# Optimization experiments

Measured on AMD Instinct MI355X. Metric: run time of the kernel, lower is better.

## Reference

```python
import jax, jax.numpy as jnp
import numpy as np

H = 256   # lstm2 hidden size
D_IN = 512  # lstm2 input size (256 fed-back out + 256 audio)
BN_EPS = 1e-5


def _lstm_cell(x, h, c, Wih, Whh, bih, bhh):
    # torch gate order: i, f, g, o
    z = x @ Wih.T + h @ Whh.T + bih + bhh  # (B, 4H)
    i, f, g, o = jnp.split(z, 4, axis=-1)
    i = jax.nn.sigmoid(i)
    f = jax.nn.sigmoid(f)
    g = jnp.tanh(g)
    o = jax.nn.sigmoid(o)
    c = f * c + i * g
    h = o * jnp.tanh(c)
    return h, c


def setup_inputs() -> dict:
    key = jax.random.key(0)
    ks = jax.random.split(key, 16)
    B, T, L = 256, 512, 16
    s = 0.05
    inp = {
        "rt": jax.random.normal(ks[0], (B, H), jnp.float32),
        "audio": jax.random.normal(ks[1], (B, T, H), jnp.float32),
        "s_rt": jax.random.normal(ks[2], (B, L, H), jnp.float32),
        # lstm2 layer 0
        "W_ih_l0": jax.random.normal(ks[3], (4 * H, D_IN), jnp.float32) * s,
        "W_hh_l0": jax.random.normal(ks[4], (4 * H, H), jnp.float32) * s,
        "b_ih_l0": jax.random.normal(ks[5], (4 * H,), jnp.float32) * s,
        "b_hh_l0": jax.random.normal(ks[6], (4 * H,), jnp.float32) * s,
        # lstm2 layer 1
        "W_ih_l1": jax.random.normal(ks[7], (4 * H, H), jnp.float32) * s,
        "W_hh_l1": jax.random.normal(ks[8], (4 * H, H), jnp.float32) * s,
        "b_ih_l1": jax.random.normal(ks[9], (4 * H,), jnp.float32) * s,
        "b_hh_l1": jax.random.normal(ks[10], (4 * H,), jnp.float32) * s,
        # rt_linear head: Linear(256,128) -> BN(128) -> ReLU -> Linear(128,6)
        "W1": jax.random.normal(ks[11], (128, H), jnp.float32) * s,
        "b1": jax.random.normal(ks[12], (128,), jnp.float32) * s,
        "gamma": jnp.ones((128,), jnp.float32),
        "beta": jnp.zeros((128,), jnp.float32),
        "W2": jax.random.normal(ks[13], (6, 128), jnp.float32) * s,
        "b2": jax.random.normal(ks[14], (6,), jnp.float32) * s,
        "max_len": 0,
    }
    return inp


def reference(rt, audio, s_rt,
              W_ih_l0, W_hh_l0, b_ih_l0, b_hh_l0,
              W_ih_l1, W_hh_l1, b_ih_l1, b_hh_l1,
              W1, b1, gamma, beta, W2, b2, max_len):
    B, T, _ = audio.shape
    prev_out = jnp.mean(s_rt, axis=1)  # (B, 256): torch.mean(s_rt, dim=1)
    h1 = c1 = h2 = c2 = jnp.zeros((B, H), audio.dtype)

    def step(carry, a_t):
        prev_out, h1, c1, h2, c2 = carry
        x = jnp.concatenate([prev_out, a_t], axis=-1)  # (B, 512)
        h1n, c1n = _lstm_cell(x, h1, c1, W_ih_l0, W_hh_l0, b_ih_l0, b_hh_l0)
        h2n, c2n = _lstm_cell(h1n, h2, c2, W_ih_l1, W_hh_l1, b_ih_l1, b_hh_l1)
        return (h2n, h1n, c1n, h2n, c2n), h2n

    audio_tm = jnp.transpose(audio, (1, 0, 2))  # (T, B, 256) time-major
    _, out_tm = jax.lax.scan(step, (prev_out, h1, c1, h2, c2), audio_tm)
    out = jnp.transpose(out_tm, (1, 0, 2)).reshape(-1, H)  # (B*T, 256)

    # rt_linear head, BatchNorm1d in training mode (batch stats)
    y = out @ W1.T + b1  # (B*T, 128)
    mu = jnp.mean(y, axis=0)
    var = jnp.var(y, axis=0)
    y = (y - mu) * jax.lax.rsqrt(var + BN_EPS) * gamma + beta
    y = jax.nn.relu(y)
    y = y @ W2.T + b2  # (B*T, 6)
    return y.reshape(B, T, -1)
```

## Files before the change

kernel.cpp:

```cpp
#include <hip/hip_runtime.h>
#include <stdint.h>

typedef unsigned int u32;
typedef unsigned short u16;
typedef unsigned long long u64;
typedef _Float16 f16;
typedef _Float16 h2_t __attribute__((ext_vector_type(2)));
typedef _Float16 f16x4 __attribute__((ext_vector_type(4)));
typedef _Float16 f16x8 __attribute__((ext_vector_type(8)));
typedef float f32x4 __attribute__((ext_vector_type(4)));
typedef float f32x16 __attribute__((ext_vector_type(16)));
typedef u32 u32x4 __attribute__((ext_vector_type(4)));

#define TT 512
#define NF 128
#define NTOT (256 * TT)

#define OFF_WA0   0u
#define OFF_WA1   1572864u
#define OFF_WAH   2621440u
#define OFF_GSUM  2883584u
#define OFF_GSQ   2884096u
#define OFF_CTR   2884608u
#define OFF_GH1   2886656u
#define OFF_GH2   3017728u
#define OFF_Y     3148800u

__device__ __forceinline__ float sigf(float x) { return 1.0f / (1.0f + __expf(-x)); }
__device__ __forceinline__ float tanh_fast(float x) { return 1.0f - 2.0f / (__expf(2.0f * x) + 1.0f); }

__global__ void prep_kernel(const float* __restrict__ Wih0, const float* __restrict__ Whh0,
                            const float* __restrict__ Wih1, const float* __restrict__ Whh1,
                            const float* __restrict__ W1,
                            f16* __restrict__ WA0, f16* __restrict__ WA1, f16* __restrict__ WAH,
                            float* __restrict__ gz, u32* __restrict__ ctr) {
    int idx = blockIdx.x * 256 + threadIdx.x;
    const int n0 = 786432, n1 = 524288, n2 = 131072;
    if (idx < n0) {
        int u = idx >> 9, r9 = idx & 511;
        int lane = r9 >> 3, j = r9 & 7;
        int ks = u % 6; u /= 6;
        int wv = u & 7, w = u >> 3;
        int lr = lane & 31, h = lane >> 5;
        int r = ((lr >> 3) << 8) + 8 * w + (lr & 7);
        int seg = ks >> 1, sig = ks & 1;
        int c = 256 * seg + 32 * wv + 16 * sig + 8 * h + j;
        float v = (c < 512) ? Wih0[r * 512 + c] : Whh0[r * 256 + (c - 512)];
        WA0[idx] = (f16)v;
    } else if (idx < n0 + n1) {
        int i2 = idx - n0;
        int lane = (i2 >> 3) & 63, j = i2 & 7;
        int ks = (i2 >> 9) & 3, wv = (i2 >> 11) & 7, w = i2 >> 14;
        int lr = lane & 31, h = lane >> 5;
        int r = ((lr >> 3) << 8) + 8 * w + (lr & 7);
        int sig = ks & 1;
        int c = 32 * wv + 16 * sig + 8 * h + j;
        float v = (ks >> 1) ? Whh1[r * 256 + c] : Wih1[r * 256 + c];
        WA1[i2] = (f16)v;
    } else if (idx < n0 + n1 + n2) {
        int i2 = idx - n0 - n1;
        int u = i2 >> 9, r9 = i2 & 511;
        int lane = r9 >> 3, j = r9 & 7;
        int ks = u & 7, w = u >> 3;
        int m = lane & 15, hh = lane >> 4;
        int k = 32 * ks + 8 * hh + j;
        float v = (m < 4) ? W1[(4 * w + m) * 256 + k] : 0.f;
        WAH[i2] = (f16)v;
    } else if (idx < n0 + n1 + n2 + 256) {
        gz[idx - n0 - n1 - n2] = 0.f;
    } else if (idx < n0 + n1 + n2 + 256 + 512) {
        ctr[idx - n0 - n1 - n2 - 256] = 0u;
    }
}

#define MFMA32L(A, BP, C) (C) = __builtin_amdgcn_mfma_f32_32x32x16_f16( \
    __builtin_bit_cast(f16x8, (A)), __builtin_bit_cast(f16x8, *(const uint4*)(BP)), (C), 0, 0, 0)
#define MFMA32R(A, B, C) (C) = __builtin_amdgcn_mfma_f32_32x32x16_f16( \
    __builtin_bit_cast(f16x8, (A)), __builtin_bit_cast(f16x8, (B)), (C), 0, 0, 0)

#define ZZWR(KW, C) do { \
    f32x4 v0_ = {(C)[0], (C)[1], (C)[2], (C)[3]};    *(f32x4*)&zz[KW][n32][4 * h32] = v0_; \
    f32x4 v1_ = {(C)[4], (C)[5], (C)[6], (C)[7]};    *(f32x4*)&zz[KW][n32][8 + 4 * h32] = v1_; \
    f32x4 v2_ = {(C)[8], (C)[9], (C)[10], (C)[11]};  *(f32x4*)&zz[KW][n32][16 + 4 * h32] = v2_; \
    f32x4 v3_ = {(C)[12], (C)[13], (C)[14], (C)[15]}; *(f32x4*)&zz[KW][n32][24 + 4 * h32] = v3_; } while (0)

#define GATHER2(F0, F1, P0, P1) asm volatile( \
    "global_load_dwordx4 %0, %2, off sc0 sc1\n\t" \
    "global_load_dwordx4 %1, %3, off sc0 sc1\n\t" \
    "s_waitcnt vmcnt(0)" \
    : "=&v"(F0), "=&v"(F1) : "v"(P0), "v"(P1) : "memory")

#define PUBX4(PTR, DATA) asm volatile( \
    "global_store_dwordx4 %0, %1, off sc0 sc1" :: "v"(PTR), "v"(DATA) : "memory")

#define HEAD_BODY(TIDX) do { \
    f32x4 C_ = {}; \
    _Pragma("unroll") \
    for (int ks_ = 0; ks_ < 8; ++ks_) \
        C_ = __builtin_amdgcn_mfma_f32_16x16x32_f16( \
            __builtin_bit_cast(f16x8, ah[ks_]), \
            __builtin_bit_cast(f16x8, \
                *(const uint4*)&Xh2[wv * 16 + (lane & 15)][32 * ks_ + 8 * ((lane >> 4) & 3)]), \
            C_, 0, 0, 0); \
    if (lane < 16) { \
        float y0 = C_[0] + b1s[0], y1 = C_[1] + b1s[1]; \
        float y2 = C_[2] + b1s[2], y3 = C_[3] + b1s[3]; \
        ys0 += y0; yq0 += y0 * y0; ys1 += y1; yq1 += y1 * y1; \
        ys2 += y2; yq2 += y2 * y2; ys3 += y3; yq3 += y3 * y3; \
        f16x4 yp; yp[0] = (f16)y0; yp[1] = (f16)y1; yp[2] = (f16)y2; yp[3] = (f16)y3; \
        int b_ = wv * 16 + lane; \
        ((u64*)ybuf)[((size_t)(g * 32 + b_) * 512 + (TIDX)) * 32 + w] = __builtin_bit_cast(u64, yp); \
    } } while (0)

#define CELL_PUB(BCS, CSTATE, SRC) do { \
    float z0 = BCS[cj], z1 = BCS[8 + cj], z2 = BCS[16 + cj], z3 = BCS[24 + cj]; \
    _Pragma("unroll") \
    for (int kw_ = 0; kw_ < 8; ++kw_) { \
        z0 += zz[kw_][cb][cj];      z1 += zz[kw_][cb][8 + cj]; \
        z2 += zz[kw_][cb][16 + cj]; z3 += zz[kw_][cb][24 + cj]; \
    } \
    float c_ = sigf(z1) * (CSTATE) + sigf(z0) * tanh_fast(z2); \
    (CSTATE) = c_; \
    f16 hf_ = (f16)(sigf(z3) * tanh_fast(c_)); \
    u32 hb_ = (u32)__builtin_bit_cast(u16, hf_); \
    u32 p01_ = hb_ | ((u32)__shfl_xor((int)hb_, 1, 64) << 16); \
    u32 p23_ = (u32)__shfl_xor((int)p01_, 2, 64); \
    u32 p45_ = (u32)__shfl_xor((int)p01_, 4, 64); \
    u32 p67_ = (u32)__shfl_xor((int)p23_, 4, 64); \
    if (cj == 0) { \
        u32x4 word_ = {p01_, p23_, p45_, p67_}; \
        PUBX4((void*)((SRC) + ((cb << 5) + w) * 2), word_); \
    } } while (0)

#define FUNNEL_SYNC(LF, CTRP, T) do { \
    asm volatile("s_waitcnt vmcnt(0)" ::: "memory"); \
    if (lane == 0) \
        __hip_atomic_fetch_add(&(LF), 1u, __ATOMIC_RELAXED, __HIP_MEMORY_SCOPE_WORKGROUP); \
    if (wv == 7 && lane == 0) { \
        int gu_ = 0; \
        while (__hip_atomic_load(&(LF), __ATOMIC_RELAXED, __HIP_MEMORY_SCOPE_WORKGROUP) < 4u * (T) \
               && ++gu_ < 100000000) {} \
        __hip_atomic_fetch_add((CTRP), 1u, __ATOMIC_RELAXED, __HIP_MEMORY_SCOPE_AGENT); \
        gu_ = 0; \
        while (__hip_atomic_load((CTRP), __ATOMIC_RELAXED, __HIP_MEMORY_SCOPE_AGENT) < 32u * (T) \
               && ++gu_ < 100000000) {} \
    } } while (0)

__global__ __launch_bounds__(512) void lstm_group_kernel(
    const float* __restrict__ audio, const float* __restrict__ s_rt,
    const uint4* __restrict__ WA0, const uint4* __restrict__ WA1, const uint4* __restrict__ WAH,
    const float* __restrict__ bih0, const float* __restrict__ bhh0,
    const float* __restrict__ bih1, const float* __restrict__ bhh1,
    const float* __restrict__ b1, u32* __restrict__ ctr,
    u64* __restrict__ gh1u, u64* __restrict__ gh2u,
    f16* __restrict__ ybuf, float* __restrict__ gsum, float* __restrict__ gsq)
{
    __shared__ __align__(16) f16 Xa[32][264];
    __shared__ __align__(16) f16 Xh2[32][264];
    __shared__ float zz[8][32][36];
    __shared__ float bc0s[32], bc1s[32], b1s[4];
    __shared__ u32 lflag[2];
    __shared__ float pad_[2700];

    const int tid = threadIdx.x;
    const int w = blockIdx.x >> 3;
    const int g = blockIdx.x & 7;
    const int wv = tid >> 6;
    const int lane = tid & 63;
    const int n32 = lane & 31;
    const int h32 = (lane >> 5) & 1;
    const int ct = tid - 256;
    const int cb = ct >> 3, cj = ct & 7;
    const int bg = tid >> 6, aq = tid & 63;

    if (tid == 0) { volatile float* vp = pad_; vp[0] = 0.f; lflag[0] = 0u; lflag[1] = 0u; }

    u32* const ctr1 = ctr + (g * 2 + 0) * 32;
    u32* const ctr2 = ctr + (g * 2 + 1) * 32;
    u64* const src1 = gh1u + (size_t)g * 2048;
    u64* const src2 = gh2u + (size_t)g * 2048;
    const size_t gbase = (size_t)n32 * 64 + 8 * wv + 2 * h32;
    const float4* const a4 = (const float4*)audio;

    uint4 a0[6], a1[4], ah[8] = {};
    #pragma unroll
    for (int ks = 0; ks < 6; ++ks) a0[ks] = WA0[((w * 8 + wv) * 6 + ks) * 64 + lane];
    #pragma unroll
    for (int ks = 0; ks < 4; ++ks) a1[ks] = WA1[((w * 8 + wv) * 4 + ks) * 64 + lane];
    if (wv < 2) {
        #pragma unroll
        for (int ks = 0; ks < 8; ++ks) ah[ks] = WAH[(w * 8 + ks) * 64 + lane];
    }

    if (tid < 32) {
        int r = ((tid >> 3) << 8) + 8 * w + (tid & 7);
        bc0s[tid] = bih0[r] + bhh0[r];
        bc1s[tid] = bih1[r] + bhh1[r];
    }
    if (tid < 4) b1s[tid] = b1[4 * w + tid];

    for (int it = tid; it < 32 * 256; it += 512) {
        int b = it >> 8, c = it & 255;
        const float* sp = s_rt + ((size_t)(32 * g + b) * 16) * 256 + c;
        float s = 0.f;
        #pragma unroll
        for (int l = 0; l < 16; ++l) s += sp[l * 256];
        Xh2[b][c] = (f16)(s * 0.0625f);
        Xa[b][c] = (f16)audio[((size_t)(32 * g + b) * 512) * 256 + c];
    }
    float4 av[8];
    if (wv < 4) {
        #pragma unroll
        for (int s = 0; s < 8; ++s)
            av[s] = a4[(size_t)(32 * g + 8 * bg + s) * 32768 + 64 + aq];
    }
    __syncthreads();

    u32x4 f20 = *(const u32x4*)&Xh2[n32][32 * wv + 8 * h32];
    u32x4 f21 = *(const u32x4*)&Xh2[n32][32 * wv + 16 + 8 * h32];
    u32x4 f10 = {0, 0, 0, 0}, f11 = {0, 0, 0, 0};
    f32x16 aAcc = {};
    MFMA32L(a0[2], &Xa[n32][32 * wv + 8 * h32], aAcc);
    MFMA32L(a0[3], &Xa[n32][32 * wv + 16 + 8 * h32], aAcc);

    float c1 = 0.f, c2 = 0.f;
    float ys0 = 0, ys1 = 0, ys2 = 0, ys3 = 0, yq0 = 0, yq1 = 0, yq2 = 0, yq3 = 0;

    for (int t = 0; t < TT; ++t) {
        const u32 T = (u32)(t + 1);
        MFMA32R(a0[0], f20, aAcc);
        MFMA32R(a0[1], f21, aAcc);
        ZZWR(wv, aAcc);
        __syncthreads();

        f32x16 Dacc = {};
        if (wv >= 4) {
            CELL_PUB(bc0s, c1, src1);
            if (t > 0) { MFMA32R(a1[2], f20, Dacc); MFMA32R(a1[3], f21, Dacc); }
            FUNNEL_SYNC(lflag[0], ctr1, T);
        } else {
            if (t > 0) { MFMA32R(a1[2], f20, Dacc); MFMA32R(a1[3], f21, Dacc); }
            if (wv < 2 && t > 0) HEAD_BODY(t - 1);
            if (t + 1 < TT) {
                #pragma unroll
                for (int s = 0; s < 8; ++s) {
                    h2_t p0_; p0_.x = (f16)av[s].x; p0_.y = (f16)av[s].y;
                    h2_t p1_; p1_.x = (f16)av[s].z; p1_.y = (f16)av[s].w;
                    uint2 pv_;
                    pv_.x = __builtin_bit_cast(u32, p0_);
                    pv_.y = __builtin_bit_cast(u32, p1_);
                    *(uint2*)&Xa[8 * bg + s][4 * aq] = pv_;
                }
            }
        }
        __syncthreads();

        GATHER2(f10, f11, (const void*)(src1 + gbase), (const void*)(src1 + gbase + 4));
        if (wv < 4 && t + 2 < TT) {
            #pragma unroll
            for (int s = 0; s < 8; ++s)
                av[s] = a4[(size_t)(32 * g + 8 * bg + s) * 32768 + (size_t)(t + 2) * 64 + aq];
        }
        MFMA32R(a1[0], f10, Dacc);
        MFMA32R(a1[1], f11, Dacc);
        ZZWR(wv, Dacc);
        __syncthreads();

        aAcc = (f32x16){};
        if (wv >= 4) {
            CELL_PUB(bc1s, c2, src2);
            if (t + 1 < TT) {
                MFMA32L(a0[2], &Xa[n32][32 * wv + 8 * h32], aAcc);
                MFMA32L(a0[3], &Xa[n32][32 * wv + 16 + 8 * h32], aAcc);
                MFMA32R(a0[4], f10, aAcc);
                MFMA32R(a0[5], f11, aAcc);
            }
            FUNNEL_SYNC(lflag[1], ctr2, T);
        } else {
            if (t + 1 < TT) {
                MFMA32L(a0[2], &Xa[n32][32 * wv + 8 * h32], aAcc);
                MFMA32L(a0[3], &Xa[n32][32 * wv + 16 + 8 * h32], aAcc);
                MFMA32R(a0[4], f10, aAcc);
                MFMA32R(a0[5], f11, aAcc);
            }
        }
        __syncthreads();

        GATHER2(f20, f21, (const void*)(src2 + gbase), (const void*)(src2 + gbase + 4));
        *(u32x4*)&Xh2[n32][32 * wv + 8 * h32] = f20;
        *(u32x4*)&Xh2[n32][32 * wv + 16 + 8 * h32] = f21;
    }
    __syncthreads();
    if (wv < 2) HEAD_BODY(TT - 1);
    if (wv < 2 && lane < 16) {
        #pragma unroll
        for (int m = 8; m >= 1; m >>= 1) {
            ys0 += __shfl_xor(ys0, m, 64); ys1 += __shfl_xor(ys1, m, 64);
            ys2 += __shfl_xor(ys2, m, 64); ys3 += __shfl_xor(ys3, m, 64);
            yq0 += __shfl_xor(yq0, m, 64); yq1 += __shfl_xor(yq1, m, 64);
            yq2 += __shfl_xor(yq2, m, 64); yq3 += __shfl_xor(yq3, m, 64);
        }
        if (lane == 0) {
            atomicAdd(&gsum[4 * w + 0], ys0); atomicAdd(&gsum[4 * w + 1], ys1);
            atomicAdd(&gsum[4 * w + 2], ys2); atomicAdd(&gsum[4 * w + 3], ys3);
            atomicAdd(&gsq[4 * w + 0], yq0); atomicAdd(&gsq[4 * w + 1], yq1);
            atomicAdd(&gsq[4 * w + 2], yq2); atomicAdd(&gsq[4 * w + 3], yq3);
        }
    }
}

__global__ __launch_bounds__(256) void head_kernel(
    const f16* __restrict__ ybuf, const float* __restrict__ gsum, const float* __restrict__ gsq,
    const float* __restrict__ gamma, const float* __restrict__ beta,
    const float* __restrict__ W2, const float* __restrict__ b2,
    float* __restrict__ out)
{
    __shared__ float sc[NF], sh[NF], W2s[6 * NF], b2s[6];
    const int tid = threadIdx.x;
    if (tid < NF) {
        const float invN = 1.f / (float)NTOT;
        float mu = gsum[tid] * invN;
        float var = gsq[tid] * invN - mu * mu;
        float iv = rsqrtf(var + 1e-5f);
        float s = gamma[tid] * iv;
        sc[tid] = s;
        sh[tid] = beta[tid] - mu * s;
    }
    for (int i = tid; i < 6 * NF; i += 256) W2s[i] = W2[i];
    if (tid < 6) b2s[tid] = b2[tid];
    __syncthreads();

    size_t n = (size_t)blockIdx.x * 256 + tid;
    const h2_t* yr = (const h2_t*)(ybuf + n * NF);
    float a0 = b2s[0], a1 = b2s[1], a2 = b2s[2], a3 = b2s[3], a4 = b2s[4], a5 = b2s[5];
    #pragma unroll 8
    for (int p = 0; p < 64; ++p) {
        h2_t v = yr[p];
        int f0 = 2 * p, f1 = 2 * p + 1;
        float v0 = fmaxf(fmaf((float)v.x, sc[f0], sh[f0]), 0.f);
        float v1 = fmaxf(fmaf((float)v.y, sc[f1], sh[f1]), 0.f);
        a0 = fmaf(v0, W2s[0 * NF + f0], a0); a0 = fmaf(v1, W2s[0 * NF + f1], a0);
        a1 = fmaf(v0, W2s[1 * NF + f0], a1); a1 = fmaf(v1, W2s[1 * NF + f1], a1);
        a2 = fmaf(v0, W2s[2 * NF + f0], a2); a2 = fmaf(v1, W2s[2 * NF + f1], a2);
        a3 = fmaf(v0, W2s[3 * NF + f0], a3); a3 = fmaf(v1, W2s[3 * NF + f1], a3);
        a4 = fmaf(v0, W2s[4 * NF + f0], a4); a4 = fmaf(v1, W2s[4 * NF + f1], a4);
        a5 = fmaf(v0, W2s[5 * NF + f0], a5); a5 = fmaf(v1, W2s[5 * NF + f1], a5);
    }
    float* op = out + n * 6;
    op[0] = a0; op[1] = a1; op[2] = a2; op[3] = a3; op[4] = a4; op[5] = a5;
}

extern "C" void kernel_launch(void* const* d_in, const int* in_sizes, int n_in,
                              void* d_out, int out_size, void* d_ws, size_t ws_size,
                              hipStream_t stream) {
    const float* audio = (const float*)d_in[1];
    const float* s_rt  = (const float*)d_in[2];
    const float* Wih0  = (const float*)d_in[3];
    const float* Whh0  = (const float*)d_in[4];
    const float* bih0  = (const float*)d_in[5];
    const float* bhh0  = (const float*)d_in[6];
    const float* Wih1  = (const float*)d_in[7];
    const float* Whh1  = (const float*)d_in[8];
    const float* bih1  = (const float*)d_in[9];
    const float* bhh1  = (const float*)d_in[10];
    const float* W1    = (const float*)d_in[11];
    const float* b1    = (const float*)d_in[12];
    const float* gamma = (const float*)d_in[13];
    const float* beta  = (const float*)d_in[14];
    const float* W2    = (const float*)d_in[15];
    const float* b2    = (const float*)d_in[16];

    char* ws = (char*)d_ws;
    f16* WA0    = (f16*)(ws + OFF_WA0);
    f16* WA1    = (f16*)(ws + OFF_WA1);
    f16* WAH    = (f16*)(ws + OFF_WAH);
    float* gsum = (float*)(ws + OFF_GSUM);
    float* gsq  = (float*)(ws + OFF_GSQ);
    u32* ctrp   = (u32*)(ws + OFF_CTR);
    u64* gh1u   = (u64*)(ws + OFF_GH1);
    u64* gh2u   = (u64*)(ws + OFF_GH2);
    f16* ybuf   = (f16*)(ws + OFF_Y);
    float* out  = (float*)d_out;

    prep_kernel<<<5635, 256, 0, stream>>>(Wih0, Whh0, Wih1, Whh1, W1,
                                          WA0, WA1, WAH, gsum, ctrp);

    lstm_group_kernel<<<256, 512, 0, stream>>>(audio, s_rt,
                                               (const uint4*)WA0, (const uint4*)WA1, (const uint4*)WAH,
                                               bih0, bhh0, bih1, bhh1, b1, ctrp,
                                               gh1u, gh2u, ybuf, gsum, gsq);

    head_kernel<<<NTOT / 256, 256, 0, stream>>>(ybuf, gsum, gsq, gamma, beta, W2, b2, out);
}
```

Baseline: 2.970 ms.

## Split batch group into two staggered halves to overlap layer-0 and layer-1 sync

Each 32-row batch group is split into two 16-row halves (X and Y) that run out of phase, so while one half computes layer 0 the other computes layer 1. Each half-layer gets its own global counter and state buffer. The single funnel wave that both signalled and polled is replaced by dedicated poller waves and split signal/wait roles. The aim is to hide the cross-workgroup barrier latency on the recurrent critical path behind useful MFMA work. In exchange, half the MFMA lanes (rows 16-31) do wasted work, there are more barriers per step, and the synchronization protocol is more complex and easier to deadlock or get wrong.

```diff
diff --git a/kernel.cpp b/kernel.cpp
--- a/kernel.cpp
+++ b/kernel.cpp
@@ -22,9 +22,8 @@
 #define OFF_GSUM  2883584u
 #define OFF_GSQ   2884096u
 #define OFF_CTR   2884608u
-#define OFF_GH1   2886656u
-#define OFF_GH2   3017728u
-#define OFF_Y     3148800u
+#define OFF_GH    2888704u
+#define OFF_Y     3150848u
 
 __device__ __forceinline__ float sigf(float x) { return 1.0f / (1.0f + __expf(-x)); }
 __device__ __forceinline__ float tanh_fast(float x) { return 1.0f - 2.0f / (__expf(2.0f * x) + 1.0f); }
@@ -68,7 +67,7 @@
         WAH[i2] = (f16)v;
     } else if (idx < n0 + n1 + n2 + 256) {
         gz[idx - n0 - n1 - n2] = 0.f;
-    } else if (idx < n0 + n1 + n2 + 256 + 512) {
+    } else if (idx < n0 + n1 + n2 + 256 + 1024) {
         ctr[idx - n0 - n1 - n2 - 256] = 0u;
     }
 }
@@ -78,11 +77,11 @@
 #define MFMA32R(A, B, C) (C) = __builtin_amdgcn_mfma_f32_32x32x16_f16( \
     __builtin_bit_cast(f16x8, (A)), __builtin_bit_cast(f16x8, (B)), (C), 0, 0, 0)
 
-#define ZZWR(KW, C) do { \
-    f32x4 v0_ = {(C)[0], (C)[1], (C)[2], (C)[3]};    *(f32x4*)&zz[KW][n32][4 * h32] = v0_; \
-    f32x4 v1_ = {(C)[4], (C)[5], (C)[6], (C)[7]};    *(f32x4*)&zz[KW][n32][8 + 4 * h32] = v1_; \
-    f32x4 v2_ = {(C)[8], (C)[9], (C)[10], (C)[11]};  *(f32x4*)&zz[KW][n32][16 + 4 * h32] = v2_; \
-    f32x4 v3_ = {(C)[12], (C)[13], (C)[14], (C)[15]}; *(f32x4*)&zz[KW][n32][24 + 4 * h32] = v3_; } while (0)
+#define ZZWRC(ZB, C) do { if (n32 < 16) { \
+    f32x4 v0_ = {(C)[0], (C)[1], (C)[2], (C)[3]};    *(f32x4*)&zz[wv][(ZB) + n32][4 * h32] = v0_; \
+    f32x4 v1_ = {(C)[4], (C)[5], (C)[6], (C)[7]};    *(f32x4*)&zz[wv][(ZB) + n32][8 + 4 * h32] = v1_; \
+    f32x4 v2_ = {(C)[8], (C)[9], (C)[10], (C)[11]};  *(f32x4*)&zz[wv][(ZB) + n32][16 + 4 * h32] = v2_; \
+    f32x4 v3_ = {(C)[12], (C)[13], (C)[14], (C)[15]}; *(f32x4*)&zz[wv][(ZB) + n32][24 + 4 * h32] = v3_; } } while (0)
 
 #define GATHER2(F0, F1, P0, P1) asm volatile( \
     "global_load_dwordx4 %0, %2, off sc0 sc1\n\t" \
@@ -90,34 +89,32 @@
     "s_waitcnt vmcnt(0)" \
     : "=&v"(F0), "=&v"(F1) : "v"(P0), "v"(P1) : "memory")
 
+#define GATHER4(F0, F1, F2, F3, P0, P1, P2, P3) asm volatile( \
+    "global_load_dwordx4 %0, %4, off sc0 sc1\n\t" \
+    "global_load_dwordx4 %1, %5, off sc0 sc1\n\t" \
+    "global_load_dwordx4 %2, %6, off sc0 sc1\n\t" \
+    "global_load_dwordx4 %3, %7, off sc0 sc1\n\t" \
+    "s_waitcnt vmcnt(0)" \
+    : "=&v"(F0), "=&v"(F1), "=&v"(F2), "=&v"(F3) \
+    : "v"(P0), "v"(P1), "v"(P2), "v"(P3) : "memory")
+
 #define PUBX4(PTR, DATA) asm volatile( \
     "global_store_dwordx4 %0, %1, off sc0 sc1" :: "v"(PTR), "v"(DATA) : "memory")
 
-#define HEAD_BODY(TIDX) do { \
-    f32x4 C_ = {}; \
-    _Pragma("unroll") \
-    for (int ks_ = 0; ks_ < 8; ++ks_) \
-        C_ = __builtin_amdgcn_mfma_f32_16x16x32_f16( \
-            __builtin_bit_cast(f16x8, ah[ks_]), \
-            __builtin_bit_cast(f16x8, \
-                *(const uint4*)&Xh2[wv * 16 + (lane & 15)][32 * ks_ + 8 * ((lane >> 4) & 3)]), \
-            C_, 0, 0, 0); \
-    if (lane < 16) { \
-        float y0 = C_[0] + b1s[0], y1 = C_[1] + b1s[1]; \
-        float y2 = C_[2] + b1s[2], y3 = C_[3] + b1s[3]; \
-        ys0 += y0; yq0 += y0 * y0; ys1 += y1; yq1 += y1 * y1; \
-        ys2 += y2; yq2 += y2 * y2; ys3 += y3; yq3 += y3 * y3; \
-        f16x4 yp; yp[0] = (f16)y0; yp[1] = (f16)y1; yp[2] = (f16)y2; yp[3] = (f16)y3; \
-        int b_ = wv * 16 + lane; \
-        ((u64*)ybuf)[((size_t)(g * 32 + b_) * 512 + (TIDX)) * 32 + w] = __builtin_bit_cast(u64, yp); \
-    } } while (0)
-
-#define CELL_PUB(BCS, CSTATE, SRC) do { \
+#define POLL(CTRP, TGT) do { int gu_ = 0; \
+    while (__hip_atomic_load((CTRP), __ATOMIC_RELAXED, __HIP_MEMORY_SCOPE_AGENT) < (TGT) \
+           && ++gu_ < 200000000) {} } while (0)
+
+#define LWAIT(LF, TGT) do { int gu_ = 0; \
+    while (__hip_atomic_load(&(LF), __ATOMIC_RELAXED, __HIP_MEMORY_SCOPE_WORKGROUP) < (TGT) \
+           && ++gu_ < 200000000) {} } while (0)
+
+#define CELLP(BCS, CSTATE, SRC, ZB) do { \
     float z0 = BCS[cj], z1 = BCS[8 + cj], z2 = BCS[16 + cj], z3 = BCS[24 + cj]; \
     _Pragma("unroll") \
     for (int kw_ = 0; kw_ < 8; ++kw_) { \
-        z0 += zz[kw_][cb][cj];      z1 += zz[kw_][cb][8 + cj]; \
-        z2 += zz[kw_][cb][16 + cj]; z3 += zz[kw_][cb][24 + cj]; \
+        z0 += zz[kw_][(ZB) + cb][cj];      z1 += zz[kw_][(ZB) + cb][8 + cj]; \
+        z2 += zz[kw_][(ZB) + cb][16 + cj]; z3 += zz[kw_][(ZB) + cb][24 + cj]; \
     } \
     float c_ = sigf(z1) * (CSTATE) + sigf(z0) * tanh_fast(z2); \
     (CSTATE) = c_; \
@@ -129,21 +126,28 @@
     u32 p67_ = (u32)__shfl_xor((int)p23_, 4, 64); \
     if (cj == 0) { \
         u32x4 word_ = {p01_, p23_, p45_, p67_}; \
-        PUBX4((void*)((SRC) + ((cb << 5) + w) * 2), word_); \
+        PUBX4((void*)((SRC) + (cb * 64 + 2 * w)), word_); \
     } } while (0)
 
-#define FUNNEL_SYNC(LF, CTRP, T) do { \
-    asm volatile("s_waitcnt vmcnt(0)" ::: "memory"); \
-    if (lane == 0) \
-        __hip_atomic_fetch_add(&(LF), 1u, __ATOMIC_RELAXED, __HIP_MEMORY_SCOPE_WORKGROUP); \
-    if (wv == 7 && lane == 0) { \
-        int gu_ = 0; \
-        while (__hip_atomic_load(&(LF), __ATOMIC_RELAXED, __HIP_MEMORY_SCOPE_WORKGROUP) < 4u * (T) \
-               && ++gu_ < 100000000) {} \
-        __hip_atomic_fetch_add((CTRP), 1u, __ATOMIC_RELAXED, __HIP_MEMORY_SCOPE_AGENT); \
-        gu_ = 0; \
-        while (__hip_atomic_load((CTRP), __ATOMIC_RELAXED, __HIP_MEMORY_SCOPE_AGENT) < 32u * (T) \
-               && ++gu_ < 100000000) {} \
+#define DRAIN() asm volatile("s_waitcnt vmcnt(0)" ::: "memory")
+
+#define HEADC(XB, BB, TIDX) do { \
+    f32x4 C_ = {}; \
+    _Pragma("unroll") \
+    for (int ks_ = 0; ks_ < 8; ++ks_) \
+        C_ = __builtin_amdgcn_mfma_f32_16x16x32_f16( \
+            __builtin_bit_cast(f16x8, ah[ks_]), \
+            __builtin_bit_cast(f16x8, \
+                *(const uint4*)&XB[lane & 15][32 * ks_ + 8 * ((lane >> 4) & 3)]), \
+            C_, 0, 0, 0); \
+    if (lane < 16) { \
+        float y0 = C_[0] + b1s[0], y1 = C_[1] + b1s[1]; \
+        float y2 = C_[2] + b1s[2], y3 = C_[3] + b1s[3]; \
+        ys0 += y0; yq0 += y0 * y0; ys1 += y1; yq1 += y1 * y1; \
+        ys2 += y2; yq2 += y2 * y2; ys3 += y3; yq3 += y3 * y3; \
+        f16x4 yp; yp[0] = (f16)y0; yp[1] = (f16)y1; yp[2] = (f16)y2; yp[3] = (f16)y3; \
+        int b_ = (BB) + lane; \
+        ((u64*)ybuf)[((size_t)(g * 32 + b_) * 512 + (TIDX)) * 32 + w] = __builtin_bit_cast(u64, yp); \
     } } while (0)
 
 __global__ __launch_bounds__(512) void lstm_group_kernel(
@@ -151,15 +155,14 @@
     const uint4* __restrict__ WA0, const uint4* __restrict__ WA1, const uint4* __restrict__ WAH,
     const float* __restrict__ bih0, const float* __restrict__ bhh0,
     const float* __restrict__ bih1, const float* __restrict__ bhh1,
-    const float* __restrict__ b1, u32* __restrict__ ctr,
-    u64* __restrict__ gh1u, u64* __restrict__ gh2u,
+    const float* __restrict__ b1, u32* __restrict__ ctr, u64* __restrict__ gh,
     f16* __restrict__ ybuf, float* __restrict__ gsum, float* __restrict__ gsq)
 {
-    __shared__ __align__(16) f16 Xa[32][264];
-    __shared__ __align__(16) f16 Xh2[32][264];
+    __shared__ __align__(16) f16 XaX[16][264], XaY[16][264];
+    __shared__ __align__(16) f16 Xh2X[16][264], Xh2Y[16][264];
     __shared__ float zz[8][32][36];
     __shared__ float bc0s[32], bc1s[32], b1s[4];
-    __shared__ u32 lflag[2];
+    __shared__ u32 lflag[4];
     __shared__ float pad_[2700];
 
     const int tid = threadIdx.x;
@@ -169,17 +172,23 @@
     const int lane = tid & 63;
     const int n32 = lane & 31;
     const int h32 = (lane >> 5) & 1;
-    const int ct = tid - 256;
-    const int cb = ct >> 3, cj = ct & 7;
-    const int bg = tid >> 6, aq = tid & 63;
-
-    if (tid == 0) { volatile float* vp = pad_; vp[0] = 0.f; lflag[0] = 0u; lflag[1] = 0u; }
-
-    u32* const ctr1 = ctr + (g * 2 + 0) * 32;
-    u32* const ctr2 = ctr + (g * 2 + 1) * 32;
-    u64* const src1 = gh1u + (size_t)g * 2048;
-    u64* const src2 = gh2u + (size_t)g * 2048;
-    const size_t gbase = (size_t)n32 * 64 + 8 * wv + 2 * h32;
+    const int cb = (tid & 127) >> 3;
+    const int cj = tid & 7;
+
+    if (tid == 0) {
+        volatile float* vp = pad_; vp[0] = 0.f;
+        lflag[0] = lflag[1] = lflag[2] = lflag[3] = 0u;
+    }
+
+    u32* const ctrX1 = ctr + (g * 4 + 0) * 32;
+    u32* const ctrX2 = ctr + (g * 4 + 1) * 32;
+    u32* const ctrY1 = ctr + (g * 4 + 2) * 32;
+    u32* const ctrY2 = ctr + (g * 4 + 3) * 32;
+    u64* const srcX1 = gh + (size_t)(g * 4 + 0) * 1024;
+    u64* const srcX2 = gh + (size_t)(g * 4 + 1) * 1024;
+    u64* const srcY1 = gh + (size_t)(g * 4 + 2) * 1024;
+    u64* const srcY2 = gh + (size_t)(g * 4 + 3) * 1024;
+    const size_t gb = (size_t)(n32 & 15) * 64 + 8 * wv + 2 * h32;
     const float4* const a4 = (const float4*)audio;
 
     uint4 a0[6], a1[4], ah[8] = {};
@@ -191,7 +200,6 @@
         #pragma unroll
         for (int ks = 0; ks < 8; ++ks) ah[ks] = WAH[(w * 8 + ks) * 64 + lane];
     }
-
     if (tid < 32) {
         int r = ((tid >> 3) << 8) + 8 * w + (tid & 7);
         bc0s[tid] = bih0[r] + bhh0[r];
@@ -205,93 +213,188 @@
         float s = 0.f;
         #pragma unroll
         for (int l = 0; l < 16; ++l) s += sp[l * 256];
-        Xh2[b][c] = (f16)(s * 0.0625f);
-        Xa[b][c] = (f16)audio[((size_t)(32 * g + b) * 512) * 256 + c];
-    }
-    float4 av[8];
-    if (wv < 4) {
-        #pragma unroll
-        for (int s = 0; s < 8; ++s)
-            av[s] = a4[(size_t)(32 * g + 8 * bg + s) * 32768 + 64 + aq];
+        f16 po = (f16)(s * 0.0625f);
+        f16 au = (f16)audio[((size_t)(32 * g + b) * 512) * 256 + c];
+        if (b < 16) { Xh2X[b][c] = po; XaX[b][c] = au; }
+        else        { Xh2Y[b - 16][c] = po; XaY[b - 16][c] = au; }
     }
     __syncthreads();
 
-    u32x4 f20 = *(const u32x4*)&Xh2[n32][32 * wv + 8 * h32];
-    u32x4 f21 = *(const u32x4*)&Xh2[n32][32 * wv + 16 + 8 * h32];
-    u32x4 f10 = {0, 0, 0, 0}, f11 = {0, 0, 0, 0};
-    f32x16 aAcc = {};
-    MFMA32L(a0[2], &Xa[n32][32 * wv + 8 * h32], aAcc);
-    MFMA32L(a0[3], &Xa[n32][32 * wv + 16 + 8 * h32], aAcc);
+    u32x4 f20X = *(const u32x4*)&Xh2X[n32 & 15][32 * wv + 8 * h32];
+    u32x4 f21X = *(const u32x4*)&Xh2X[n32 & 15][32 * wv + 16 + 8 * h32];
+    u32x4 f20Y = *(const u32x4*)&Xh2Y[n32 & 15][32 * wv + 8 * h32];
+    u32x4 f21Y = *(const u32x4*)&Xh2Y[n32 & 15][32 * wv + 16 + 8 * h32];
+    u32x4 f10X = {0, 0, 0, 0}, f11X = {0, 0, 0, 0};
+    u32x4 f10Y = {0, 0, 0, 0}, f11Y = {0, 0, 0, 0};
+    float4 avX[8], avY[8];
 
     float c1 = 0.f, c2 = 0.f;
     float ys0 = 0, ys1 = 0, ys2 = 0, ys3 = 0, yq0 = 0, yq1 = 0, yq2 = 0, yq3 = 0;
 
     for (int t = 0; t < TT; ++t) {
         const u32 T = (u32)(t + 1);
-        MFMA32R(a0[0], f20, aAcc);
-        MFMA32R(a0[1], f21, aAcc);
-        ZZWR(wv, aAcc);
+        if (t > 0) {
+            GATHER4(f20X, f21X, f10Y, f11Y,
+                    (const void*)(srcX2 + gb), (const void*)(srcX2 + gb + 4),
+                    (const void*)(srcY1 + gb), (const void*)(srcY1 + gb + 4));
+            if (n32 < 16) {
+                *(u32x4*)&Xh2X[n32][32 * wv + 8 * h32] = f20X;
+                *(u32x4*)&Xh2X[n32][32 * wv + 16 + 8 * h32] = f21X;
+            }
+        }
+        if ((wv == 2 || wv == 3) && t + 1 < TT) {
+            #pragma unroll
+            for (int s = 0; s < 8; ++s)
+                avX[s] = a4[(size_t)(32 * g + (wv - 2) * 8 + s) * 32768 + (size_t)(t + 1) * 64 + lane];
+        }
+        {
+            f32x16 aXF = {};
+            MFMA32R(a0[0], f20X, aXF); MFMA32R(a0[1], f21X, aXF);
+            MFMA32L(a0[2], &XaX[n32 & 15][32 * wv + 8 * h32], aXF);
+            MFMA32L(a0[3], &XaX[n32 & 15][32 * wv + 16 + 8 * h32], aXF);
+            MFMA32R(a0[4], f10X, aXF); MFMA32R(a0[5], f11X, aXF);
+            ZZWRC(0, aXF);
+            f32x16 aYD = {};
+            if (t > 0) {
+                MFMA32R(a1[0], f10Y, aYD); MFMA32R(a1[1], f11Y, aYD);
+                if (t > 1) { MFMA32R(a1[2], f20Y, aYD); MFMA32R(a1[3], f21Y, aYD); }
+            }
+            ZZWRC(16, aYD);
+        }
         __syncthreads();
-
-        f32x16 Dacc = {};
-        if (wv >= 4) {
-            CELL_PUB(bc0s, c1, src1);
-            if (t > 0) { MFMA32R(a1[2], f20, Dacc); MFMA32R(a1[3], f21, Dacc); }
-            FUNNEL_SYNC(lflag[0], ctr1, T);
+        if (wv == 4 || wv == 5) {
+            CELLP(bc0s, c1, srcX1, 0);
+            DRAIN();
+            if (lane == 0) __hip_atomic_fetch_add(&lflag[0], 1u, __ATOMIC_RELAXED, __HIP_MEMORY_SCOPE_WORKGROUP);
+            if (tid == 256) {
+                LWAIT(lflag[0], 2u * T);
+                __hip_atomic_fetch_add(ctrX1, 1u, __ATOMIC_RELAXED, __HIP_MEMORY_SCOPE_AGENT);
+            }
+        } else if (wv >= 6) {
+            if (t > 0) {
+                CELLP(bc1s, c2, srcY2, 16);
+                DRAIN();
+                if (lane == 0) __hip_atomic_fetch_add(&lflag[1], 1u, __ATOMIC_RELAXED, __HIP_MEMORY_SCOPE_WORKGROUP);
+                if (tid == 384) {
+                    LWAIT(lflag[1], 2u * (u32)t);
+                    __hip_atomic_fetch_add(ctrY2, 1u, __ATOMIC_RELAXED, __HIP_MEMORY_SCOPE_AGENT);
+                }
+            }
+        } else if (wv == 0) {
+            if (t > 0) HEADC(Xh2X, 0, t - 1);
+            if (lane == 0) POLL(ctrX1, 32u * T);
+        } else if (wv == 1) {
+            if (lane == 0) POLL(ctrY2, 32u * (u32)t);
         } else {
-            if (t > 0) { MFMA32R(a1[2], f20, Dacc); MFMA32R(a1[3], f21, Dacc); }
-            if (wv < 2 && t > 0) HEAD_BODY(t - 1);
+            if (t > 0) {
+                #pragma unroll
+                for (int s = 0; s < 8; ++s) {
+                    h2_t p0_; p0_.x = (f16)avY[s].x; p0_.y = (f16)avY[s].y;
+                    h2_t p1_; p1_.x = (f16)avY[s].z; p1_.y = (f16)avY[s].w;
+                    uint2 pv_; pv_.x = __builtin_bit_cast(u32, p0_); pv_.y = __builtin_bit_cast(u32, p1_);
+                    *(uint2*)&XaY[(wv - 2) * 8 + s][4 * lane] = pv_;
+                }
+            }
+        }
+        __syncthreads();
+        if (t > 0) {
+            GATHER4(f10X, f11X, f20Y, f21Y,
+                    (const void*)(srcX1 + gb), (const void*)(srcX1 + gb + 4),
+                    (const void*)(srcY2 + gb), (const void*)(srcY2 + gb + 4));
+            if (n32 < 16) {
+                *(u32x4*)&Xh2Y[n32][32 * wv + 8 * h32] = f20Y;
+                *(u32x4*)&Xh2Y[n32][32 * wv + 16 + 8 * h32] = f21Y;
+            }
+        } else {
+            GATHER2(f10X, f11X, (const void*)(srcX1 + gb), (const void*)(srcX1 + gb + 4));
+        }
+        if ((wv == 2 || wv == 3) && t + 1 < TT) {
+            #pragma unroll
+            for (int s = 0; s < 8; ++s)
+                avY[s] = a4[(size_t)(32 * g + 16 + (wv - 2) * 8 + s) * 32768 + (size_t)(t + 1) * 64 + lane];
+        }
+        {
+            f32x16 aXD = {};
+            MFMA32R(a1[0], f10X, aXD); MFMA32R(a1[1], f11X, aXD);
+            if (t > 0) { MFMA32R(a1[2], f20X, aXD); MFMA32R(a1[3], f21X, aXD); }
+            ZZWRC(0, aXD);
+            f32x16 aYF = {};
+            MFMA32R(a0[0], f20Y, aYF); MFMA32R(a0[1], f21Y, aYF);
+            MFMA32L(a0[2], &XaY[n32 & 15][32 * wv + 8 * h32], aYF);
+            MFMA32L(a0[3], &XaY[n32 & 15][32 * wv + 16 + 8 * h32], aYF);
+            MFMA32R(a0[4], f10Y, aYF); MFMA32R(a0[5], f11Y, aYF);
+            ZZWRC(16, aYF);
+        }
+        __syncthreads();
+        if (wv == 4 || wv == 5) {
+            CELLP(bc1s, c2, srcX2, 0);
+            DRAIN();
+            if (lane == 0) __hip_atomic_fetch_add(&lflag[2], 1u, __ATOMIC_RELAXED, __HIP_MEMORY_SCOPE_WORKGROUP);
+            if (tid == 256) {
+                LWAIT(lflag[2], 2u * T);
+                __hip_atomic_fetch_add(ctrX2, 1u, __ATOMIC_RELAXED, __HIP_MEMORY_SCOPE_AGENT);
+            }
+        } else if (wv >= 6) {
+            CELLP(bc0s, c1, srcY1, 16);
+            DRAIN();
+            if (lane == 0) __hip_atomic_fetch_add(&lflag[3], 1u, __ATOMIC_RELAXED, __HIP_MEMORY_SCOPE_WORKGROUP);
+            if (tid == 384) {
+                LWAIT(lflag[3], 2u * T);
+                __hip_atomic_fetch_add(ctrY1, 1u, __ATOMIC_RELAXED, __HIP_MEMORY_SCOPE_AGENT);
+            }
+        } else if (wv == 0) {
+            if (lane == 0) POLL(ctrX2, 32u * T);
+        } else if (wv == 1) {
+            if (t > 0) HEADC(Xh2Y, 16, t - 1);
+            if (lane == 0) POLL(ctrY1, 32u * T);
+        } else {
             if (t + 1 < TT) {
                 #pragma unroll
                 for (int s = 0; s < 8; ++s) {
-                    h2_t p0_; p0_.x = (f16)av[s].x; p0_.y = (f16)av[s].y;
-                    h2_t p1_; p1_.x = (f16)av[s].z; p1_.y = (f16)av[s].w;
-                    uint2 pv_;
-                    pv_.x = __builtin_bit_cast(u32, p0_);
-                    pv_.y = __builtin_bit_cast(u32, p1_);
-                    *(uint2*)&Xa[8 * bg + s][4 * aq] = pv_;
+                    h2_t p0_; p0_.x = (f16)avX[s].x; p0_.y = (f16)avX[s].y;
+                    h2_t p1_; p1_.x = (f16)avX[s].z; p1_.y = (f16)avX[s].w;
+                    uint2 pv_; pv_.x = __builtin_bit_cast(u32, p0_); pv_.y = __builtin_bit_cast(u32, p1_);
+                    *(uint2*)&XaX[(wv - 2) * 8 + s][4 * lane] = pv_;
                 }
             }
         }
         __syncthreads();
-
-        GATHER2(f10, f11, (const void*)(src1 + gbase), (const void*)(src1 + gbase + 4));
-        if (wv < 4 && t + 2 < TT) {
-            #pragma unroll
-            for (int s = 0; s < 8; ++s)
-                av[s] = a4[(size_t)(32 * g + 8 * bg + s) * 32768 + (size_t)(t + 2) * 64 + aq];
-        }
-        MFMA32R(a1[0], f10, Dacc);
-        MFMA32R(a1[1], f11, Dacc);
-        ZZWR(wv, Dacc);
-        __syncthreads();
-
-        aAcc = (f32x16){};
-        if (wv >= 4) {
-            CELL_PUB(bc1s, c2, src2);
-            if (t + 1 < TT) {
-                MFMA32L(a0[2], &Xa[n32][32 * wv + 8 * h32], aAcc);
-                MFMA32L(a0[3], &Xa[n32][32 * wv + 16 + 8 * h32], aAcc);
-                MFMA32R(a0[4], f10, aAcc);
-                MFMA32R(a0[5], f11, aAcc);
-            }
-            FUNNEL_SYNC(lflag[1], ctr2, T);
-        } else {
-            if (t + 1 < TT) {
-                MFMA32L(a0[2], &Xa[n32][32 * wv + 8 * h32], aAcc);
-                MFMA32L(a0[3], &Xa[n32][32 * wv + 16 + 8 * h32], aAcc);
-                MFMA32R(a0[4], f10, aAcc);
-                MFMA32R(a0[5], f11, aAcc);
-            }
-        }
-        __syncthreads();
-
-        GATHER2(f20, f21, (const void*)(src2 + gbase), (const void*)(src2 + gbase + 4));
-        *(u32x4*)&Xh2[n32][32 * wv + 8 * h32] = f20;
-        *(u32x4*)&Xh2[n32][32 * wv + 16 + 8 * h32] = f21;
+    }
+    GATHER4(f20X, f21X, f10Y, f11Y,
+            (const void*)(srcX2 + gb), (const void*)(srcX2 + gb + 4),
+            (const void*)(srcY1 + gb), (const void*)(srcY1 + gb + 4));
+    if (n32 < 16) {
+        *(u32x4*)&Xh2X[n32][32 * wv + 8 * h32] = f20X;
+        *(u32x4*)&Xh2X[n32][32 * wv + 16 + 8 * h32] = f21X;
+    }
+    {
+        f32x16 aYD = {};
+        MFMA32R(a1[0], f10Y, aYD); MFMA32R(a1[1], f11Y, aYD);
+        MFMA32R(a1[2], f20Y, aYD); MFMA32R(a1[3], f21Y, aYD);
+        ZZWRC(16, aYD);
     }
     __syncthreads();
-    if (wv < 2) HEAD_BODY(TT - 1);
+    if (wv >= 6) {
+        CELLP(bc1s, c2, srcY2, 16);
+        DRAIN();
+        if (lane == 0) __hip_atomic_fetch_add(&lflag[1], 1u, __ATOMIC_RELAXED, __HIP_MEMORY_SCOPE_WORKGROUP);
+        if (tid == 384) {
+            LWAIT(lflag[1], 2u * (u32)TT);
+            __hip_atomic_fetch_add(ctrY2, 1u, __ATOMIC_RELAXED, __HIP_MEMORY_SCOPE_AGENT);
+        }
+    } else if (wv == 0) {
+        HEADC(Xh2X, 0, TT - 1);
+    } else if (wv == 1) {
+        if (lane == 0) POLL(ctrY2, 32u * (u32)TT);
+    }
+    __syncthreads();
+    GATHER2(f20Y, f21Y, (const void*)(srcY2 + gb), (const void*)(srcY2 + gb + 4));
+    if (n32 < 16) {
+        *(u32x4*)&Xh2Y[n32][32 * wv + 8 * h32] = f20Y;
+        *(u32x4*)&Xh2Y[n32][32 * wv + 16 + 8 * h32] = f21Y;
+    }
+    __syncthreads();
+    if (wv == 1) HEADC(Xh2Y, 16, TT - 1);
     if (wv < 2 && lane < 16) {
         #pragma unroll
         for (int m = 8; m >= 1; m >>= 1) {
@@ -377,18 +480,17 @@
     float* gsum = (float*)(ws + OFF_GSUM);
     float* gsq  = (float*)(ws + OFF_GSQ);
     u32* ctrp   = (u32*)(ws + OFF_CTR);
-    u64* gh1u   = (u64*)(ws + OFF_GH1);
-    u64* gh2u   = (u64*)(ws + OFF_GH2);
+    u64* ghp    = (u64*)(ws + OFF_GH);
     f16* ybuf   = (f16*)(ws + OFF_Y);
     float* out  = (float*)d_out;
 
-    prep_kernel<<<5635, 256, 0, stream>>>(Wih0, Whh0, Wih1, Whh1, W1,
+    prep_kernel<<<5637, 256, 0, stream>>>(Wih0, Whh0, Wih1, Whh1, W1,
                                           WA0, WA1, WAH, gsum, ctrp);
 
     lstm_group_kernel<<<256, 512, 0, stream>>>(audio, s_rt,
                                                (const uint4*)WA0, (const uint4*)WA1, (const uint4*)WAH,
-                                               bih0, bhh0, bih1, bhh1, b1, ctrp,
-                                               gh1u, gh2u, ybuf, gsum, gsq);
+                                               bih0, bhh0, bih1, bhh1, b1, ctrp, ghp,
+                                               ybuf, gsum, gsq);
 
     head_kernel<<<NTOT / 256, 256, 0, stream>>>(ybuf, gsum, gsq, gamma, beta, W2, b2, out);
 }
```

Measured after the change: 6.335 ms. 2.13x slower.

## Replace atomic group barriers with time-tagged hidden-state words polled by readers

Applied to the files above, without the earlier changes.

Each published fp16 hidden value is now packed with its timestep in the upper 16 bits of a 32-bit word. Consumers poll their own slice until every tag matches the current step, which removes the per-step workgroup and agent-scope atomic counter barriers (FUNNEL_SYNC). The prep kernel now zeroes the tagged hidden-state buffers instead of the counters. The audio prefetch for step t+2 is moved after the second gather. The exchange traffic doubles, and readers spin with s_sleep on global loads instead of waiting on a single counter.

```diff
diff --git a/kernel.cpp b/kernel.cpp
--- a/kernel.cpp
+++ b/kernel.cpp
@@ -21,10 +21,9 @@
 #define OFF_WAH   2621440u
 #define OFF_GSUM  2883584u
 #define OFF_GSQ   2884096u
-#define OFF_CTR   2884608u
-#define OFF_GH1   2886656u
-#define OFF_GH2   3017728u
-#define OFF_Y     3148800u
+#define OFF_GH1   2884608u
+#define OFF_GH2   3146752u
+#define OFF_Y     3408896u
 
 __device__ __forceinline__ float sigf(float x) { return 1.0f / (1.0f + __expf(-x)); }
 __device__ __forceinline__ float tanh_fast(float x) { return 1.0f - 2.0f / (__expf(2.0f * x) + 1.0f); }
@@ -33,7 +32,7 @@
                             const float* __restrict__ Wih1, const float* __restrict__ Whh1,
                             const float* __restrict__ W1,
                             f16* __restrict__ WA0, f16* __restrict__ WA1, f16* __restrict__ WAH,
-                            float* __restrict__ gz, u32* __restrict__ ctr) {
+                            float* __restrict__ gz, u32* __restrict__ ghz) {
     int idx = blockIdx.x * 256 + threadIdx.x;
     const int n0 = 786432, n1 = 524288, n2 = 131072;
     if (idx < n0) {
@@ -68,8 +67,8 @@
         WAH[i2] = (f16)v;
     } else if (idx < n0 + n1 + n2 + 256) {
         gz[idx - n0 - n1 - n2] = 0.f;
-    } else if (idx < n0 + n1 + n2 + 256 + 512) {
-        ctr[idx - n0 - n1 - n2 - 256] = 0u;
+    } else if (idx < n0 + n1 + n2 + 256 + 131072) {
+        ghz[idx - n0 - n1 - n2 - 256] = 0u;
     }
 }
 
@@ -84,14 +83,45 @@
     f32x4 v2_ = {(C)[8], (C)[9], (C)[10], (C)[11]};  *(f32x4*)&zz[KW][n32][16 + 4 * h32] = v2_; \
     f32x4 v3_ = {(C)[12], (C)[13], (C)[14], (C)[15]}; *(f32x4*)&zz[KW][n32][24 + 4 * h32] = v3_; } while (0)
 
-#define GATHER2(F0, F1, P0, P1) asm volatile( \
-    "global_load_dwordx4 %0, %2, off sc0 sc1\n\t" \
-    "global_load_dwordx4 %1, %3, off sc0 sc1\n\t" \
-    "s_waitcnt vmcnt(0)" \
-    : "=&v"(F0), "=&v"(F1) : "v"(P0), "v"(P1) : "memory")
-
 #define PUBX4(PTR, DATA) asm volatile( \
     "global_store_dwordx4 %0, %1, off sc0 sc1" :: "v"(PTR), "v"(DATA) : "memory")
+
+#define LOAD4T(W0, W1, W2, W3, B) asm volatile( \
+    "global_load_dwordx4 %0, %4, off sc0 sc1\n\t" \
+    "global_load_dwordx4 %1, %5, off sc0 sc1\n\t" \
+    "global_load_dwordx4 %2, %6, off sc0 sc1\n\t" \
+    "global_load_dwordx4 %3, %7, off sc0 sc1\n\t" \
+    "s_waitcnt vmcnt(0)" \
+    : "=&v"(W0), "=&v"(W1), "=&v"(W2), "=&v"(W3) \
+    : "v"(B), "v"((B) + 4), "v"((B) + 16), "v"((B) + 20) : "memory")
+
+#define TGATHER(F0, F1, BASE, T) do { \
+    const u32* b_ = (BASE); \
+    u32x4 w0_, w1_, w2_, w3_; \
+    LOAD4T(w0_, w1_, w2_, w3_, b_); \
+    int gu_ = 0; \
+    while (true) { \
+        u32 st_ = ((w0_.x >> 16) ^ (T)) | ((w0_.y >> 16) ^ (T)) \
+                | ((w0_.z >> 16) ^ (T)) | ((w0_.w >> 16) ^ (T)) \
+                | ((w1_.x >> 16) ^ (T)) | ((w1_.y >> 16) ^ (T)) \
+                | ((w1_.z >> 16) ^ (T)) | ((w1_.w >> 16) ^ (T)) \
+                | ((w2_.x >> 16) ^ (T)) | ((w2_.y >> 16) ^ (T)) \
+                | ((w2_.z >> 16) ^ (T)) | ((w2_.w >> 16) ^ (T)) \
+                | ((w3_.x >> 16) ^ (T)) | ((w3_.y >> 16) ^ (T)) \
+                | ((w3_.z >> 16) ^ (T)) | ((w3_.w >> 16) ^ (T)); \
+        if (st_ == 0 || ++gu_ > 200000) break; \
+        __builtin_amdgcn_s_sleep(1); \
+        LOAD4T(w0_, w1_, w2_, w3_, b_); \
+    } \
+    (F0).x = (w0_.x & 0xffffu) | (w0_.y << 16); \
+    (F0).y = (w0_.z & 0xffffu) | (w0_.w << 16); \
+    (F0).z = (w1_.x & 0xffffu) | (w1_.y << 16); \
+    (F0).w = (w1_.z & 0xffffu) | (w1_.w << 16); \
+    (F1).x = (w2_.x & 0xffffu) | (w2_.y << 16); \
+    (F1).y = (w2_.z & 0xffffu) | (w2_.w << 16); \
+    (F1).z = (w3_.x & 0xffffu) | (w3_.y << 16); \
+    (F1).w = (w3_.z & 0xffffu) | (w3_.w << 16); \
+} while (0)
 
 #define HEAD_BODY(TIDX) do { \
     f32x4 C_ = {}; \
@@ -112,7 +142,7 @@
         ((u64*)ybuf)[((size_t)(g * 32 + b_) * 512 + (TIDX)) * 32 + w] = __builtin_bit_cast(u64, yp); \
     } } while (0)
 
-#define CELL_PUB(BCS, CSTATE, SRC) do { \
+#define CELLPT(BCS, CSTATE, SRC, TG) do { \
     float z0 = BCS[cj], z1 = BCS[8 + cj], z2 = BCS[16 + cj], z3 = BCS[24 + cj]; \
     _Pragma("unroll") \
     for (int kw_ = 0; kw_ < 8; ++kw_) { \
@@ -122,28 +152,13 @@
     float c_ = sigf(z1) * (CSTATE) + sigf(z0) * tanh_fast(z2); \
     (CSTATE) = c_; \
     f16 hf_ = (f16)(sigf(z3) * tanh_fast(c_)); \
-    u32 hb_ = (u32)__builtin_bit_cast(u16, hf_); \
-    u32 p01_ = hb_ | ((u32)__shfl_xor((int)hb_, 1, 64) << 16); \
-    u32 p23_ = (u32)__shfl_xor((int)p01_, 2, 64); \
-    u32 p45_ = (u32)__shfl_xor((int)p01_, 4, 64); \
-    u32 p67_ = (u32)__shfl_xor((int)p23_, 4, 64); \
-    if (cj == 0) { \
-        u32x4 word_ = {p01_, p23_, p45_, p67_}; \
-        PUBX4((void*)((SRC) + ((cb << 5) + w) * 2), word_); \
-    } } while (0)
-
-#define FUNNEL_SYNC(LF, CTRP, T) do { \
-    asm volatile("s_waitcnt vmcnt(0)" ::: "memory"); \
-    if (lane == 0) \
-        __hip_atomic_fetch_add(&(LF), 1u, __ATOMIC_RELAXED, __HIP_MEMORY_SCOPE_WORKGROUP); \
-    if (wv == 7 && lane == 0) { \
-        int gu_ = 0; \
-        while (__hip_atomic_load(&(LF), __ATOMIC_RELAXED, __HIP_MEMORY_SCOPE_WORKGROUP) < 4u * (T) \
-               && ++gu_ < 100000000) {} \
-        __hip_atomic_fetch_add((CTRP), 1u, __ATOMIC_RELAXED, __HIP_MEMORY_SCOPE_AGENT); \
-        gu_ = 0; \
-        while (__hip_atomic_load((CTRP), __ATOMIC_RELAXED, __HIP_MEMORY_SCOPE_AGENT) < 32u * (T) \
-               && ++gu_ < 100000000) {} \
+    u32 tw_ = ((TG) << 16) | (u32)__builtin_bit_cast(u16, hf_); \
+    u32 t1_ = (u32)__shfl_xor((int)tw_, 1, 64); \
+    u32 t2_ = (u32)__shfl_xor((int)tw_, 2, 64); \
+    u32 t3_ = (u32)__shfl_xor((int)tw_, 3, 64); \
+    if ((cj & 3) == 0) { \
+        u32x4 word_ = {tw_, t1_, t2_, t3_}; \
+        PUBX4((void*)((SRC) + (cb * 256 + 8 * w + cj)), word_); \
     } } while (0)
 
 __global__ __launch_bounds__(512) void lstm_group_kernel(
@@ -151,15 +166,14 @@
     const uint4* __restrict__ WA0, const uint4* __restrict__ WA1, const uint4* __restrict__ WAH,
     const float* __restrict__ bih0, const float* __restrict__ bhh0,
     const float* __restrict__ bih1, const float* __restrict__ bhh1,
-    const float* __restrict__ b1, u32* __restrict__ ctr,
-    u64* __restrict__ gh1u, u64* __restrict__ gh2u,
+    const float* __restrict__ b1,
+    u32* __restrict__ gh1, u32* __restrict__ gh2,
     f16* __restrict__ ybuf, float* __restrict__ gsum, float* __restrict__ gsq)
 {
     __shared__ __align__(16) f16 Xa[32][264];
     __shared__ __align__(16) f16 Xh2[32][264];
     __shared__ float zz[8][32][36];
     __shared__ float bc0s[32], bc1s[32], b1s[4];
-    __shared__ u32 lflag[2];
     __shared__ float pad_[2700];
 
     const int tid = threadIdx.x;
@@ -173,13 +187,12 @@
     const int cb = ct >> 3, cj = ct & 7;
     const int bg = tid >> 6, aq = tid & 63;
 
-    if (tid == 0) { volatile float* vp = pad_; vp[0] = 0.f; lflag[0] = 0u; lflag[1] = 0u; }
-
-    u32* const ctr1 = ctr + (g * 2 + 0) * 32;
-    u32* const ctr2 = ctr + (g * 2 + 1) * 32;
-    u64* const src1 = gh1u + (size_t)g * 2048;
-    u64* const src2 = gh2u + (size_t)g * 2048;
-    const size_t gbase = (size_t)n32 * 64 + 8 * wv + 2 * h32;
+    if (tid == 0) { volatile float* vp = pad_; vp[0] = 0.f; }
+
+    u32* const src1 = gh1 + (size_t)g * 8192;
+    u32* const src2 = gh2 + (size_t)g * 8192;
+    const u32* const gb1 = src1 + (size_t)n32 * 256 + 32 * wv + 8 * h32;
+    const u32* const gb2 = src2 + (size_t)n32 * 256 + 32 * wv + 8 * h32;
     const float4* const a4 = (const float4*)audio;
 
     uint4 a0[6], a1[4], ah[8] = {};
@@ -191,7 +204,6 @@
         #pragma unroll
         for (int ks = 0; ks < 8; ++ks) ah[ks] = WAH[(w * 8 + ks) * 64 + lane];
     }
-
     if (tid < 32) {
         int r = ((tid >> 3) << 8) + 8 * w + (tid & 7);
         bc0s[tid] = bih0[r] + bhh0[r];
@@ -235,9 +247,8 @@
 
         f32x16 Dacc = {};
         if (wv >= 4) {
-            CELL_PUB(bc0s, c1, src1);
+            CELLPT(bc0s, c1, src1, T);
             if (t > 0) { MFMA32R(a1[2], f20, Dacc); MFMA32R(a1[3], f21, Dacc); }
-            FUNNEL_SYNC(lflag[0], ctr1, T);
         } else {
             if (t > 0) { MFMA32R(a1[2], f20, Dacc); MFMA32R(a1[3], f21, Dacc); }
             if (wv < 2 && t > 0) HEAD_BODY(t - 1);
@@ -255,12 +266,7 @@
         }
         __syncthreads();
 
-        GATHER2(f10, f11, (const void*)(src1 + gbase), (const void*)(src1 + gbase + 4));
-        if (wv < 4 && t + 2 < TT) {
-            #pragma unroll
-            for (int s = 0; s < 8; ++s)
-                av[s] = a4[(size_t)(32 * g + 8 * bg + s) * 32768 + (size_t)(t + 2) * 64 + aq];
-        }
+        TGATHER(f10, f11, gb1, T);
         MFMA32R(a1[0], f10, Dacc);
         MFMA32R(a1[1], f11, Dacc);
         ZZWR(wv, Dacc);
@@ -268,14 +274,13 @@
 
         aAcc = (f32x16){};
         if (wv >= 4) {
-            CELL_PUB(bc1s, c2, src2);
+            CELLPT(bc1s, c2, src2, T);
             if (t + 1 < TT) {
                 MFMA32L(a0[2], &Xa[n32][32 * wv + 8 * h32], aAcc);
                 MFMA32L(a0[3], &Xa[n32][32 * wv + 16 + 8 * h32], aAcc);
                 MFMA32R(a0[4], f10, aAcc);
                 MFMA32R(a0[5], f11, aAcc);
             }
-            FUNNEL_SYNC(lflag[1], ctr2, T);
         } else {
             if (t + 1 < TT) {
                 MFMA32L(a0[2], &Xa[n32][32 * wv + 8 * h32], aAcc);
@@ -286,9 +291,14 @@
         }
         __syncthreads();
 
-        GATHER2(f20, f21, (const void*)(src2 + gbase), (const void*)(src2 + gbase + 4));
+        TGATHER(f20, f21, gb2, T);
         *(u32x4*)&Xh2[n32][32 * wv + 8 * h32] = f20;
         *(u32x4*)&Xh2[n32][32 * wv + 16 + 8 * h32] = f21;
+        if (wv < 4 && t + 2 < TT) {
+            #pragma unroll
+            for (int s = 0; s < 8; ++s)
+                av[s] = a4[(size_t)(32 * g + 8 * bg + s) * 32768 + (size_t)(t + 2) * 64 + aq];
+        }
     }
     __syncthreads();
     if (wv < 2) HEAD_BODY(TT - 1);
@@ -376,19 +386,18 @@
     f16* WAH    = (f16*)(ws + OFF_WAH);
     float* gsum = (float*)(ws + OFF_GSUM);
     float* gsq  = (float*)(ws + OFF_GSQ);
-    u32* ctrp   = (u32*)(ws + OFF_CTR);
-    u64* gh1u   = (u64*)(ws + OFF_GH1);
-    u64* gh2u   = (u64*)(ws + OFF_GH2);
+    u32* gh1    = (u32*)(ws + OFF_GH1);
+    u32* gh2    = (u32*)(ws + OFF_GH2);
     f16* ybuf   = (f16*)(ws + OFF_Y);
     float* out  = (float*)d_out;
 
-    prep_kernel<<<5635, 256, 0, stream>>>(Wih0, Whh0, Wih1, Whh1, W1,
-                                          WA0, WA1, WAH, gsum, ctrp);
+    prep_kernel<<<6145, 256, 0, stream>>>(Wih0, Whh0, Wih1, Whh1, W1,
+                                          WA0, WA1, WAH, gsum, gh1);
 
     lstm_group_kernel<<<256, 512, 0, stream>>>(audio, s_rt,
                                                (const uint4*)WA0, (const uint4*)WA1, (const uint4*)WAH,
-                                               bih0, bhh0, bih1, bhh1, b1, ctrp,
-                                               gh1u, gh2u, ybuf, gsum, gsq);
+                                               bih0, bhh0, bih1, bhh1, b1,
+                                               gh1, gh2, ybuf, gsum, gsq);
 
     head_kernel<<<NTOT / 256, 256, 0, stream>>>(ybuf, gsum, gsq, gamma, beta, W2, b2, out);
 }
```

Result: slower. 4.381 ms (+47.5%).
